# Optimization experiments

Hardware: AMD Instinct MI355X
Metric: run time of the kernel (lower is better)

The kernel has to match this reference:

```python
import jax, jax.numpy as jnp
import numpy as np

N_HEAD = 16
ROPE_BASE = 10000.0
EPS = 1e-6


def _rms_norm(x):
    return x / jnp.sqrt(jnp.mean(x * x, axis=-1, keepdims=True) + EPS)


def _rotary_cos_sin(n_pos, dim, dtype):
    # NOTE: faithful to the source, n_pos == n_head (not seq_len) because
    # Rotary.forward reads x.shape[2] of a (B,T,H,D) tensor.
    inv_freq = 1.0 / (ROPE_BASE ** (jnp.arange(0, dim, 2, dtype=jnp.float32) / dim))
    t = jnp.arange(n_pos, dtype=jnp.float32)
    freqs = jnp.outer(t, inv_freq)  # (n_pos, dim//2)
    return jnp.cos(freqs).astype(dtype)[None, None], jnp.sin(freqs).astype(dtype)[None, None]


def _apply_rotary(x, cos, sin):
    d = x.shape[-1] // 2
    x1, x2 = x[..., :d], x[..., d:]
    return jnp.concatenate([x1 * cos + x2 * sin, -x1 * sin + x2 * cos], axis=-1)


def setup_inputs() -> dict:
    key = jax.random.key(0)
    ks = jax.random.split(key, 8)
    B, T, C = 4, 1024, 2048
    x = jax.random.normal(ks[0], (B, T, C), dtype=jnp.float32)
    v1 = jax.random.normal(ks[1], (B, T, N_HEAD, C // N_HEAD), dtype=jnp.float32)
    s = 0.02
    W_qkv = jax.random.normal(ks[2], (C, 3 * C), dtype=jnp.float32) * s
    b_qkv = jax.random.normal(ks[3], (3 * C,), dtype=jnp.float32) * s
    W_proj = jax.random.normal(ks[4], (C, C), dtype=jnp.float32) * s
    b_proj = jax.random.normal(ks[5], (C,), dtype=jnp.float32) * s
    lamb = jnp.float32(0.5)
    return {"x": x, "v1": v1, "W_qkv": W_qkv, "b_qkv": b_qkv,
            "W_proj": W_proj, "b_proj": b_proj, "lamb": lamb}


def reference(x, v1, W_qkv, b_qkv, W_proj, b_proj, lamb):
    B, T, C = x.shape
    H = N_HEAD
    D = C // H
    qkv = x @ W_qkv + b_qkv  # (B,T,3C)
    q, k, v = jnp.split(qkv, 3, axis=-1)
    q = q.reshape(B, T, H, D)
    k = k.reshape(B, T, H, D)
    v = v.reshape(B, T, H, D)
    v1 = v1.reshape(B, T, H, D)
    value = (1.0 - lamb) * v + lamb * v1  # lambda value-residual mix
    q = _rms_norm(q)
    k = _rms_norm(k)
    cos, sin = _rotary_cos_sin(H, D, x.dtype)  # rotary over head axis (source bug, kept)
    q = _apply_rotary(q, cos, sin)
    k = _apply_rotary(k, cos, sin)
    # causal attention, default flex_attention scale 1/sqrt(D)
    scale = 1.0 / jnp.sqrt(jnp.float32(D)).astype(x.dtype)
    scores = jnp.einsum('bqhd,bkhd->bhqk', q, k) * scale
    causal = jnp.tril(jnp.ones((T, T), dtype=bool))
    scores = jnp.where(causal[None, None], scores, jnp.finfo(scores.dtype).min)
    probs = jax.nn.softmax(scores, axis=-1)
    attn = jnp.einsum('bhqk,bkhd->bqhd', probs, value).reshape(B, T, C)
    out = attn @ W_proj + b_proj
    return out, v1
```

## Files before the change

### kernel.cpp

```cpp
#include <hip/hip_runtime.h>
#include <stdint.h>
#include <stddef.h>

typedef unsigned short u16;
typedef __attribute__((ext_vector_type(8))) short  bf16x8;
typedef __attribute__((ext_vector_type(4))) unsigned short u16x4;
typedef __attribute__((ext_vector_type(4))) float  f32x4;

#define DEVI __device__ __forceinline__

DEVI float bf2f(u16 u){ union{uint32_t i; float f;} v; v.i = ((uint32_t)u)<<16; return v.f; }
DEVI u16 f2bf(float f){ union{float f; uint32_t i;} v; v.f=f; uint32_t r = v.i + 0x7fffu + ((v.i>>16)&1u); return (u16)(r>>16); }

DEVI void gload_lds16(const void* g, void* l){
  __builtin_amdgcn_global_load_lds((const __attribute__((address_space(1))) void*)g,
                                   (__attribute__((address_space(3))) void*)l, 16, 0, 0);
}

__global__ void k_cvt_bf16(const float* __restrict__ in, u16* __restrict__ out, int n){
  int i = (blockIdx.x*256 + threadIdx.x)*4;
  int st = gridDim.x*256*4;
  for (; i < n; i += st){
    f32x4 v = *(const f32x4*)(in + i);
    u16x4 o;
    #pragma unroll
    for (int j=0;j<4;j++) o[j] = f2bf(v[j]);
    *(u16x4*)(out + i) = o;
  }
}

__global__ __launch_bounds__(256) void k_transpose_cvt(const float* __restrict__ in, u16* __restrict__ out, int K, int N){
  __shared__ float tile[32][33];
  int nb = blockIdx.x*32, kb = blockIdx.y*32;
  int tx = threadIdx.x & 31, ty = threadIdx.x >> 5;
  #pragma unroll
  for (int i=0;i<32;i+=8)
    tile[ty+i][tx] = in[(size_t)(kb+ty+i)*N + nb+tx];
  __syncthreads();
  #pragma unroll
  for (int i=0;i<32;i+=8)
    out[(size_t)(nb+ty+i)*K + kb+tx] = f2bf(tile[tx][ty+i]);
}

#define STG_A(SLAB, GSRC) \
  gload_lds16((GSRC) + off0, (SLAB) + tid*8);
#define STG_B(SLAB, GSRC) \
  gload_lds16((GSRC) + off0, (SLAB) + tid*8); \
  gload_lds16((GSRC) + off1, (SLAB) + 4096 + tid*8);

#define RD4(SLAB, ROWBASE, DST) \
  { _Pragma("unroll") for (int f=0; f<4; f++){ \
      int row_ = (ROWBASE) + f*16 + lr; \
      int rp_ = row_>>1; \
      int slot_ = ((((row_&1)<<2) | lg) ^ (rp_&7)); \
      DST[f] = *(const bf16x8*)((const char*)(SLAB) + rp_*128 + slot_*16); } }

#define MM16(AA, BB) \
  __builtin_amdgcn_s_setprio(1); \
  { _Pragma("unroll") for (int f=0; f<4; f++) \
    { _Pragma("unroll") for (int nf=0; nf<4; nf++) \
      acc[f][nf] = __builtin_amdgcn_mfma_f32_16x16x32_bf16(AA[f], BB[nf], acc[f][nf], 0,0,0); } } \
  __builtin_amdgcn_s_setprio(0);

#define BAR_LGKM \
  __builtin_amdgcn_s_barrier(); \
  __builtin_amdgcn_sched_barrier(0); \
  asm volatile("s_waitcnt lgkmcnt(0)" ::: "memory"); \
  __builtin_amdgcn_sched_barrier(0);

#define WAITV(N) asm volatile("s_waitcnt vmcnt(" #N ")" ::: "memory");
#define ORDER_FENCE __builtin_amdgcn_sched_barrier(0); asm volatile("" ::: "memory");

template<bool OUT_BF16>
__global__ __launch_bounds__(512) void k_gemm128x256(
    const u16* __restrict__ A, const u16* __restrict__ Bt,
    const float* __restrict__ bias, void* __restrict__ Cout,
    int M, int N, int K, int nbn)
{
  __shared__ __attribute__((aligned(16))) u16 sA[3][2][4096];
  __shared__ __attribute__((aligned(16))) u16 sB[3][2][8192];
  int nwg = gridDim.x;
  int orig = blockIdx.x;
  int wgid = (orig & 7)*(nwg>>3) + (orig>>3);
  int bm = wgid / nbn, bn = wgid % nbn;
  const int tid = threadIdx.x;
  const int wid = tid>>6, l = tid&63;
  const int lr = l&15, lg = l>>4;
  const int wm = wid>>2, wn = wid&3;
  const int rba = wm*64, rbb = wn*64;

  uint32_t off0, off1;
  { int cc=tid;     int rp=cc>>3, cb=(cc&7)^(rp&7); off0 = (uint32_t)((rp*2+(cb>>2))*K + (cb&3)*8); }
  { int cc=512+tid; int rp=cc>>3, cb=(cc&7)^(rp&7); off1 = (uint32_t)((rp*2+(cb>>2))*K + (cb&3)*8); }
  const u16* Ab = A + (size_t)bm*128*K;
  const u16* Bb = Bt + (size_t)bn*256*K;

  f32x4 acc[4][4] = {};
  bf16x8 a0[4], a1[4], b0[4], b1[4];
  const int NT = K>>6;

  STG_B(&sB[0][0][0], Bb);      STG_A(&sA[0][0][0], Ab);      ORDER_FENCE;
  STG_B(&sB[0][1][0], Bb+32);   STG_A(&sA[0][1][0], Ab+32);   ORDER_FENCE;
  STG_B(&sB[1][0][0], Bb+64);   STG_A(&sA[1][0][0], Ab+64);
  WAITV(6);
  __builtin_amdgcn_s_barrier();
  __builtin_amdgcn_sched_barrier(0);

  int s0=0, s1=1, s2=2;
  for (int t=0; t<=NT-3; ++t){
    const u16* A1 = Ab + (t+1)*64;  const u16* B1 = Bb + (t+1)*64;
    const u16* A2 = Ab + (t+2)*64;  const u16* B2 = Bb + (t+2)*64;
    RD4(&sB[s0][0][0], rbb, b0); RD4(&sA[s0][0][0], rba, a0);
    STG_B(&sB[s1][1][0], B1+32); STG_A(&sA[s1][1][0], A1+32);
    WAITV(6);
    BAR_LGKM; MM16(a0, b0);
    RD4(&sB[s0][1][0], rbb, b1); RD4(&sA[s0][1][0], rba, a1);
    STG_B(&sB[s2][0][0], B2);    STG_A(&sA[s2][0][0], A2);
    WAITV(6);
    BAR_LGKM; MM16(a1, b1);
    int tmp=s0; s0=s1; s1=s2; s2=tmp;
  }
  {
    const u16* A1 = Ab + (NT-1)*64;  const u16* B1 = Bb + (NT-1)*64;
    RD4(&sB[s0][0][0], rbb, b0); RD4(&sA[s0][0][0], rba, a0);
    STG_B(&sB[s1][1][0], B1+32); STG_A(&sA[s1][1][0], A1+32);
    WAITV(6);
    BAR_LGKM; MM16(a0, b0);
    RD4(&sB[s0][1][0], rbb, b1); RD4(&sA[s0][1][0], rba, a1);
    WAITV(3);
    BAR_LGKM; MM16(a1, b1);
  }
  {
    RD4(&sB[s1][0][0], rbb, b0); RD4(&sA[s1][0][0], rba, a0);
    WAITV(0);
    BAR_LGKM; MM16(a0, b0);
    RD4(&sB[s1][1][0], rbb, b1); RD4(&sA[s1][1][0], rba, a1);
    BAR_LGKM; MM16(a1, b1);
  }

  #pragma unroll
  for (int nf=0; nf<4; nf++){
    int col = bn*256 + wn*64 + nf*16 + lr;
    float bv = bias[col];
    #pragma unroll
    for (int m=0; m<4; m++){
      #pragma unroll
      for (int j=0; j<4; j++){
        int row = bm*128 + wm*64 + m*16 + lg*4 + j;
        float v = acc[m][nf][j] + bv;
        if (OUT_BF16) ((u16*)Cout)[(size_t)row*N + col] = f2bf(v);
        else          ((float*)Cout)[(size_t)row*N + col] = v;
      }
    }
  }
}

DEVI void unpack16(const u16* p, float* f){
  bf16x8 a = *(const bf16x8*)p, b = *(const bf16x8*)(p+8);
  #pragma unroll
  for (int i=0;i<8;i++){ f[i]=bf2f((u16)a[i]); f[8+i]=bf2f((u16)b[i]); }
}

__global__ __launch_bounds__(256) void k_qkv_post(
    const u16*  __restrict__ qkv,
    const float* __restrict__ v1,
    const float* __restrict__ lambp,
    u16* __restrict__ qn,
    u16* __restrict__ kn,
    u16* __restrict__ vT,
    float* __restrict__ v1out)
{
  __shared__ float cosv[64], sinv[64];
  __shared__ __attribute__((aligned(16))) u16 sv[64][136];
  int bid = blockIdx.x;
  int tb = bid & 15, h = (bid>>4)&15, b = bid>>8;
  int tid = threadIdx.x;
  if (tid < 64){
    float ang = (float)h * exp2f(-(float)tid * 0.2076205059304595f);
    cosv[tid] = cosf(ang);
    sinv[tid] = sinf(ang);
  }
  float lamb = lambp[0];
  int row = tid>>2, p = tid&3;
  int t = tb*64 + row;
  size_t base = ((size_t)(b*1024 + t))*6144 + (size_t)h*128;
  __syncthreads();

  #pragma unroll
  for (int qc=0; qc<2; ++qc){
    const u16* src = qkv + base + qc*2048;
    u16* dst = (qc==0 ? qn : kn) + ((size_t)(b*1024+t))*2048 + h*128;
    int j0 = p*16;
    float x1[16], x2[16];
    unpack16(src + j0, x1);
    unpack16(src + 64 + j0, x2);
    float ss = 0.f;
    #pragma unroll
    for (int i=0;i<16;i++) ss += x1[i]*x1[i] + x2[i]*x2[i];
    ss += __shfl_xor(ss, 1);
    ss += __shfl_xor(ss, 2);
    float rn = rsqrtf(ss*(1.0f/128.0f) + 1e-6f);
    bf16x8 o1a,o1b,o2a,o2b;
    #pragma unroll
    for (int i=0;i<16;i++){
      float c = cosv[j0+i], s = sinv[j0+i];
      u16 a = f2bf(( x1[i]*c + x2[i]*s)*rn);
      u16 bq= f2bf((-x1[i]*s + x2[i]*c)*rn);
      if (i<8){ o1a[i]=(short)a; o2a[i]=(short)bq; } else { o1b[i-8]=(short)a; o2b[i-8]=(short)bq; }
    }
    *(bf16x8*)(dst + j0)      = o1a;
    *(bf16x8*)(dst + j0 + 8)  = o1b;
    *(bf16x8*)(dst + 64 + j0)     = o2a;
    *(bf16x8*)(dst + 64 + j0 + 8) = o2b;
  }

  {
    const u16* srcv = qkv + base + 4096;
    size_t v1off = (((size_t)(b*1024+t))*16 + h)*128;
    const float* src1 = v1 + v1off;
    float* dst1 = v1out + v1off;
    int d0 = p*32;
    #pragma unroll
    for (int c8=0;c8<4;c8++){
      bf16x8 vv = *(const bf16x8*)(srcv + d0 + c8*8);
      f32x4 a0 = *(const f32x4*)(src1 + d0 + c8*8);
      f32x4 a1 = *(const f32x4*)(src1 + d0 + c8*8 + 4);
      *(f32x4*)(dst1 + d0 + c8*8) = a0;
      *(f32x4*)(dst1 + d0 + c8*8 + 4) = a1;
      bf16x8 o;
      #pragma unroll
      for (int i=0;i<8;i++){
        float x1v = (i<4)? a0[i] : a1[i-4];
        o[i] = (short)f2bf((1.0f-lamb)*bf2f((u16)vv[i]) + lamb*x1v);
      }
      *(bf16x8*)(&sv[row][d0 + c8*8]) = o;
    }
  }
  __syncthreads();
  {
    int d = tid>>1, tc = (tid&1)*32;
    u16 tmp[32];
    #pragma unroll
    for (int i=0;i<32;i++) tmp[i] = sv[tc+i][d];
    u16* dst = vT + (((size_t)(b*16+h))*128 + d)*1024 + tb*64 + tc;
    #pragma unroll
    for (int c8=0;c8<4;c8++){
      bf16x8 o;
      #pragma unroll
      for (int i=0;i<8;i++) o[i]=(short)tmp[c8*8+i];
      *(bf16x8*)(dst + c8*8) = o;
    }
  }
}

__global__ __launch_bounds__(256) void k_attn(
    const u16* __restrict__ Q,
    const u16* __restrict__ Kn,
    const u16* __restrict__ Vt,
    u16* __restrict__ O)
{
  __shared__ __attribute__((aligned(16))) u16 sK[2][64*128];
  __shared__ __attribute__((aligned(16))) u16 sV[2][128*64];
  __shared__ __attribute__((aligned(16))) u16 sP[4][16*64];
  int bid = blockIdx.x;
  int qi = 15 - (bid>>6);
  int bh = bid & 63;
  int h = bh & 15, b = bh >> 4;
  int tid = threadIdx.x, w = tid>>6, l = tid&63, lr = l&15, lg = l>>4;
  int qrow = qi*64 + w*16;
  bf16x8 aq[4];
  {
    const u16* qp = Q + ((size_t)(b*1024 + qrow + lr))*2048 + h*128 + lg*8;
    #pragma unroll
    for (int ks=0; ks<4; ++ks) aq[ks] = *(const bf16x8*)(qp + ks*32);
  }
  f32x4 accO[8] = {};
  float mrun[4], srun[4];
  #pragma unroll
  for (int j=0;j<4;j++){ mrun[j] = -INFINITY; srun[j]=0.f; }
  const float scale = 0.08838834764831845f;
  const size_t kbase = (size_t)(b*1024)*2048 + (size_t)h*128;
  const u16* vbase = Vt + ((size_t)(b*16+h))*128*1024;

  auto STAGE = [&](int kt, int buf){
    #pragma unroll
    for (int it=0; it<4; ++it){
      int c = it*256+tid;
      int key = c>>4, d16 = (c&15)^(key&7);
      gload_lds16(Kn + kbase + (size_t)(kt*64+key)*2048 + d16*8, &sK[buf][c*8]);
    }
    #pragma unroll
    for (int it=0; it<4; ++it){
      int c = it*256+tid;
      int d = c>>3, k8 = (c&7)^(d&7);
      gload_lds16(vbase + (size_t)d*1024 + kt*64 + k8*8, &sV[buf][c*8]);
    }
  };

  STAGE(0, 0);
  int cur = 0;
  for (int kt=0; kt<=qi; ++kt){
    if (kt < qi){
      STAGE(kt+1, cur^1);
      asm volatile("s_waitcnt vmcnt(8)" ::: "memory");
    } else {
      asm volatile("s_waitcnt vmcnt(0)" ::: "memory");
    }
    __builtin_amdgcn_s_barrier();
    __builtin_amdgcn_sched_barrier(0);
    const char* kb = (const char*)sK[cur];
    const char* vb = (const char*)sV[cur];

    f32x4 accS[4] = {};
    __builtin_amdgcn_s_setprio(1);
    #pragma unroll
    for (int ks=0; ks<4; ++ks){
      #pragma unroll
      for (int n=0;n<4;n++){
        int key = n*16+lr, k = ks*32+lg*8;
        int byt = ((key<<8) + (k<<1)) ^ ((key&7)<<4);
        bf16x8 bk = *(const bf16x8*)(kb + byt);
        accS[n] = __builtin_amdgcn_mfma_f32_16x16x32_bf16(aq[ks], bk, accS[n], 0,0,0);
      }
    }
    __builtin_amdgcn_s_setprio(0);
    bool diag = (kt == qi);
    float pj[4][4];
    #pragma unroll
    for (int j=0;j<4;j++){
      int qg = qrow + lg*4 + j;
      float mx = -INFINITY;
      #pragma unroll
      for (int n=0;n<4;n++){
        float s = accS[n][j]*scale;
        if (diag && (kt*64 + n*16 + lr) > qg) s = -1e30f;
        pj[n][j] = s;
        mx = fmaxf(mx, s);
      }
      #pragma unroll
      for (int off=1; off<16; off<<=1) mx = fmaxf(mx, __shfl_xor(mx, off));
      float mnew = fmaxf(mrun[j], mx);
      float fac = __expf(mrun[j] - mnew);
      float ps = 0.f;
      #pragma unroll
      for (int n=0;n<4;n++){ float e = __expf(pj[n][j]-mnew); pj[n][j]=e; ps += e; }
      #pragma unroll
      for (int off=1; off<16; off<<=1) ps += __shfl_xor(ps, off);
      srun[j] = srun[j]*fac + ps;
      mrun[j] = mnew;
      #pragma unroll
      for (int n=0;n<8;n++) accO[n][j] *= fac;
    }
    #pragma unroll
    for (int n=0;n<4;n++)
      #pragma unroll
      for (int j=0;j<4;j++){
        int q = lg*4+j, key = n*16+lr;
        int byt = ((q<<7) + (key<<1)) ^ ((q&7)<<4);
        *(u16*)((char*)sP[w] + byt) = f2bf(pj[n][j]);
      }
    bf16x8 pA[2];
    #pragma unroll
    for (int ks=0; ks<2; ++ks){
      int k = ks*32 + lg*8;
      int byt = ((lr<<7) + (k<<1)) ^ ((lr&7)<<4);
      pA[ks] = *(const bf16x8*)((const char*)sP[w] + byt);
    }
    __builtin_amdgcn_s_setprio(1);
    #pragma unroll
    for (int ks=0; ks<2; ++ks)
      #pragma unroll
      for (int n=0;n<8;n++){
        int d = n*16+lr, k = ks*32+lg*8;
        int byt = ((d<<7) + (k<<1)) ^ ((d&7)<<4);
        bf16x8 bv = *(const bf16x8*)(vb + byt);
        accO[n] = __builtin_amdgcn_mfma_f32_16x16x32_bf16(pA[ks], bv, accO[n], 0,0,0);
      }
    __builtin_amdgcn_s_setprio(0);
    __builtin_amdgcn_s_barrier();
    cur ^= 1;
  }
  #pragma unroll
  for (int j=0;j<4;j++){
    float inv = 1.0f / srun[j];
    int row = qrow + lg*4 + j;
    u16* op = O + ((size_t)(b*1024+row))*2048 + h*128;
    #pragma unroll
    for (int n=0;n<8;n++)
      op[n*16+lr] = f2bf(accO[n][j]*inv);
  }
}

extern "C" void kernel_launch(void* const* d_in, const int* in_sizes, int n_in,
                              void* d_out, int out_size, void* d_ws, size_t ws_size,
                              hipStream_t stream)
{
  const float* x     = (const float*)d_in[0];
  const float* v1    = (const float*)d_in[1];
  const float* Wqkv  = (const float*)d_in[2];
  const float* bqkv  = (const float*)d_in[3];
  const float* Wproj = (const float*)d_in[4];
  const float* bproj = (const float*)d_in[5];
  const float* lamb  = (const float*)d_in[6];

  char* ws = (char*)d_ws;
  u16* qkv_b  = (u16*)(ws);
  u16* WqkvT  = (u16*)(ws +  50331648);
  u16* WprojT = (u16*)(ws +  75497472);
  u16* xb     = (u16*)(ws +  83886080);
  u16* vT     = xb;
  u16* qn     = (u16*)(ws + 100663296);
  u16* kn     = (u16*)(ws + 117440512);
  u16* attn_b = qkv_b;

  float* out = (float*)d_out;

  hipLaunchKernelGGL(k_cvt_bf16, dim3(2048), dim3(256), 0, stream, x, xb, 8388608);
  hipLaunchKernelGGL(k_transpose_cvt, dim3(192, 64), dim3(256), 0, stream, Wqkv,  WqkvT,  2048, 6144);
  hipLaunchKernelGGL(k_transpose_cvt, dim3(64, 64),  dim3(256), 0, stream, Wproj, WprojT, 2048, 2048);
  hipLaunchKernelGGL((k_gemm128x256<true>),  dim3(768), dim3(512), 0, stream, xb, WqkvT, bqkv, (void*)qkv_b, 4096, 6144, 2048, 24);
  hipLaunchKernelGGL(k_qkv_post, dim3(1024), dim3(256), 0, stream, qkv_b, v1, lamb, qn, kn, vT, out + 8388608);
  hipLaunchKernelGGL(k_attn, dim3(1024), dim3(256), 0, stream, qn, kn, vT, attn_b);
  hipLaunchKernelGGL((k_gemm128x256<false>), dim3(256), dim3(512), 0, stream, attn_b, WprojT, bproj, (void*)out, 4096, 2048, 2048, 8);
}
```

Before: 280.7 us.

## Fuse prep conversions into one kernel and remap GEMM tiles per XCD

Merges the input bf16 conversion and both weight transpose-converts into a single launch that dispatches on block index, removing two kernel launches. Changes the GEMM workgroup-to-tile mapping so each XCD owns a contiguous set of N column tiles across all M rows, so weight tiles are shared within an XCD's L2. This trades A-tile sharing for B-tile locality and relies on the grid being divisible as assumed.

```diff
diff --git a/kernel.cpp b/kernel.cpp
--- a/kernel.cpp
+++ b/kernel.cpp
@@ -17,22 +17,35 @@
                                    (__attribute__((address_space(3))) void*)l, 16, 0, 0);
 }
 
-__global__ void k_cvt_bf16(const float* __restrict__ in, u16* __restrict__ out, int n){
-  int i = (blockIdx.x*256 + threadIdx.x)*4;
-  int st = gridDim.x*256*4;
-  for (; i < n; i += st){
-    f32x4 v = *(const f32x4*)(in + i);
-    u16x4 o;
-    #pragma unroll
-    for (int j=0;j<4;j++) o[j] = f2bf(v[j]);
-    *(u16x4*)(out + i) = o;
-  }
-}
-
-__global__ __launch_bounds__(256) void k_transpose_cvt(const float* __restrict__ in, u16* __restrict__ out, int K, int N){
+__global__ __launch_bounds__(256) void k_prep(
+    const float* __restrict__ x,     u16* __restrict__ xb,
+    const float* __restrict__ Wqkv,  u16* __restrict__ WqkvT,
+    const float* __restrict__ Wproj, u16* __restrict__ WprojT)
+{
   __shared__ float tile[32][33];
-  int nb = blockIdx.x*32, kb = blockIdx.y*32;
-  int tx = threadIdx.x & 31, ty = threadIdx.x >> 5;
+  int bid = blockIdx.x;
+  int tid = threadIdx.x;
+  if (bid < 2048){
+    int i = (bid*256 + tid)*4;
+    const int st = 2048*256*4;
+    for (; i < 8388608; i += st){
+      f32x4 v = *(const f32x4*)(x + i);
+      u16x4 o;
+      #pragma unroll
+      for (int j=0;j<4;j++) o[j] = f2bf(v[j]);
+      *(u16x4*)(xb + i) = o;
+    }
+    return;
+  }
+  const float* in; u16* out; int K, N, nb, kb;
+  if (bid < 2048 + 12288){
+    int b2 = bid - 2048; in = Wqkv; out = WqkvT; K = 2048; N = 6144;
+    nb = (b2 % 192)*32; kb = (b2 / 192)*32;
+  } else {
+    int b3 = bid - 2048 - 12288; in = Wproj; out = WprojT; K = 2048; N = 2048;
+    nb = (b3 % 64)*32; kb = (b3 / 64)*32;
+  }
+  int tx = tid & 31, ty = tid >> 5;
   #pragma unroll
   for (int i=0;i<32;i+=8)
     tile[ty+i][tx] = in[(size_t)(kb+ty+i)*N + nb+tx];
@@ -75,14 +88,16 @@
 __global__ __launch_bounds__(512) void k_gemm128x256(
     const u16* __restrict__ A, const u16* __restrict__ Bt,
     const float* __restrict__ bias, void* __restrict__ Cout,
-    int M, int N, int K, int nbn)
+    int M, int N, int K, int nbnx)
 {
   __shared__ __attribute__((aligned(16))) u16 sA[3][2][4096];
   __shared__ __attribute__((aligned(16))) u16 sB[3][2][8192];
-  int nwg = gridDim.x;
   int orig = blockIdx.x;
-  int wgid = (orig & 7)*(nwg>>3) + (orig>>3);
-  int bm = wgid / nbn, bn = wgid % nbn;
+  int xcd = orig & 7;
+  int idx = orig >> 3;
+  int bnx = idx % nbnx;
+  int bm  = idx / nbnx;
+  int bn  = xcd*nbnx + bnx;
   const int tid = threadIdx.x;
   const int wid = tid>>6, l = tid&63;
   const int lr = l&15, lg = l>>4;
@@ -415,11 +430,10 @@
 
   float* out = (float*)d_out;
 
-  hipLaunchKernelGGL(k_cvt_bf16, dim3(2048), dim3(256), 0, stream, x, xb, 8388608);
-  hipLaunchKernelGGL(k_transpose_cvt, dim3(192, 64), dim3(256), 0, stream, Wqkv,  WqkvT,  2048, 6144);
-  hipLaunchKernelGGL(k_transpose_cvt, dim3(64, 64),  dim3(256), 0, stream, Wproj, WprojT, 2048, 2048);
-  hipLaunchKernelGGL((k_gemm128x256<true>),  dim3(768), dim3(512), 0, stream, xb, WqkvT, bqkv, (void*)qkv_b, 4096, 6144, 2048, 24);
+  hipLaunchKernelGGL(k_prep, dim3(2048+12288+4096), dim3(256), 0, stream,
+                     x, xb, Wqkv, WqkvT, Wproj, WprojT);
+  hipLaunchKernelGGL((k_gemm128x256<true>),  dim3(768), dim3(512), 0, stream, xb, WqkvT, bqkv, (void*)qkv_b, 4096, 6144, 2048, 3);
   hipLaunchKernelGGL(k_qkv_post, dim3(1024), dim3(256), 0, stream, qkv_b, v1, lamb, qn, kn, vT, out + 8388608);
   hipLaunchKernelGGL(k_attn, dim3(1024), dim3(256), 0, stream, qn, kn, vT, attn_b);
-  hipLaunchKernelGGL((k_gemm128x256<false>), dim3(256), dim3(512), 0, stream, attn_b, WprojT, bproj, (void*)out, 4096, 2048, 2048, 8);
-}
+  hipLaunchKernelGGL((k_gemm128x256<false>), dim3(256), dim3(512), 0, stream, attn_b, WprojT, bproj, (void*)out, 4096, 2048, 2048, 1);
+}
```

After: 273.1 us, median of 3. -2.7%, faster.
